# Optimization experiments

Measured on AMD Instinct MI355X. Metric: run time of the kernel, lower is better.

The kernel has to match this reference:

```python
import jax, jax.numpy as jnp
import numpy as np

B, K, D, H, T, S = 8192, 32, 768, 256, 16, 2  # batch, candidates, d_model, hidden, topics, shots
MAX_SHOT = 8
TEMP = 0.1


def _l2n(x, eps=1e-12):
    return x / jnp.clip(jnp.linalg.norm(x, axis=-1, keepdims=True), eps)


def setup_inputs() -> dict:
    key = jax.random.key(0)
    ks = jax.random.split(key, 20)
    f32 = jnp.float32
    rn = lambda k, shape, s: jax.random.normal(k, shape, f32) * s
    inp = {}
    inp['query_emb'] = jax.random.normal(ks[0], (B, D), f32)
    inp['cand_emb'] = jax.random.normal(ks[1], (B, K, D), f32)
    inp['W_in'] = rn(ks[2], (H, D), 0.03)              # input_proj (bias=False)
    inp['Wq_a'] = rn(ks[3], (H, H), 0.05)              # MHA in-proj q
    inp['Wk_a'] = rn(ks[4], (H, H), 0.05)
    inp['Wv_a'] = rn(ks[5], (H, H), 0.05)
    inp['bq_a'] = jnp.zeros((H,), f32)
    inp['bk_a'] = jnp.zeros((H,), f32)
    inp['bv_a'] = jnp.zeros((H,), f32)
    inp['Wo_a'] = rn(ks[6], (H, H), 0.05)              # MHA out-proj
    inp['bo_a'] = jnp.zeros((H,), f32)
    inp['ln_w'] = jnp.ones((H,), f32)
    inp['ln_b'] = jnp.zeros((H,), f32)
    inp['Wq'] = jnp.eye(H, dtype=f32) + rn(ks[7], (H, H), 0.01)   # query_proj (eye init + noise)
    inp['Wc'] = jnp.eye(H, dtype=f32) + rn(ks[8], (H, H), 0.01)   # cand_proj
    inp['W_ih'] = rn(ks[9], (3 * H, H), 0.05)          # GRUCell ih (r,z,n)
    inp['W_hh'] = rn(ks[10], (3 * H, H), 0.05)
    inp['b_ih'] = jnp.zeros((3 * H,), f32)
    inp['b_hh'] = jnp.zeros((3 * H,), f32)
    inp['step_emb'] = rn(ks[11], (MAX_SHOT, H), 0.02)
    inp['topic_protos'] = rn(ks[12], (T, H), 0.02)
    inp['Wqt'] = rn(ks[13], (T, H), 0.05)              # query_topic_head
    inp['bqt'] = jnp.zeros((T,), f32)
    inp['cover_lambda'] = jnp.array(-2.0, f32)
    return inp


def reference(query_emb, cand_emb, W_in, Wq_a, Wk_a, Wv_a, bq_a, bk_a, bv_a,
              Wo_a, bo_a, ln_w, ln_b, Wq, Wc, W_ih, W_hh, b_ih, b_hh,
              step_emb, topic_protos, Wqt, bqt, cover_lambda):
    Bd = query_emb.shape[0]
    # input projection 768 -> 256
    qr = query_emb @ W_in.T                                # [B,H]
    cr = jnp.einsum('bkd,hd->bkh', cand_emb, W_in)         # [B,K,H]
    # single-head cross-attention (query len 1, eval mode -> no dropout)
    q = qr @ Wq_a.T + bq_a
    k = jnp.einsum('bkh,gh->bkg', cr, Wk_a) + bk_a
    v = jnp.einsum('bkh,gh->bkg', cr, Wv_a) + bv_a
    attn = jax.nn.softmax(jnp.einsum('bh,bkh->bk', q, k) / jnp.sqrt(jnp.float32(H)))
    ctx = jnp.einsum('bk,bkh->bh', attn, v) @ Wo_a.T + bo_a
    # residual + LayerNorm
    x = ctx + qr
    mu = jnp.mean(x, -1, keepdims=True)
    var = jnp.var(x, -1, keepdims=True)
    qe = (x - mu) / jnp.sqrt(var + 1e-5) * ln_w + ln_b
    # pointer projections + L2 normalize
    h = _l2n(qe @ Wq.T)                                    # [B,H]
    cn = _l2n(jnp.einsum('bkh,gh->bkg', cr, Wc))           # [B,K,H]
    topic_probs = jax.nn.softmax(jnp.einsum('bkh,th->bkt', cn, _l2n(topic_protos)))  # [B,K,T]
    need = jax.nn.softmax(h @ Wqt.T + bqt)                 # [B,T]
    lam = jax.nn.softplus(cover_lambda)
    sel = jnp.zeros((Bd, K), bool)
    covered = jnp.zeros((Bd, T), jnp.float32)
    rows = jnp.arange(Bd)
    logits, preds = [], []
    for step in range(S):
        h_step = _l2n(h + step_emb[min(step, MAX_SHOT - 1)])
        scores = jnp.einsum('bh,bkh->bk', h_step, cn) / TEMP
        if step > 0:
            uncov = jnp.clip(1.0 - covered, 0.0, 1.0)
            gain = jnp.einsum('bt,bkt->bk', need * uncov, topic_probs)
            scores = scores + lam * gain
        scores = jnp.where(sel, -100.0, scores)
        logits.append(scores)
        idx = jnp.argmax(scores, axis=-1)                  # labels=None -> greedy feedback
        preds.append(idx)
        sel = sel.at[rows, idx].set(True)
        chosen = cn[rows, idx]                             # [B,H]
        covered = jnp.minimum(covered + topic_probs[rows, idx], 1.0)
        # GRUCell update
        gi = chosen @ W_ih.T + b_ih
        gh = h @ W_hh.T + b_hh
        ir, iz, ig = jnp.split(gi, 3, axis=-1)
        hr, hz, hg = jnp.split(gh, 3, axis=-1)
        r = jax.nn.sigmoid(ir + hr)
        z = jax.nn.sigmoid(iz + hz)
        n = jnp.tanh(ig + r * hg)
        h = _l2n((1.0 - z) * n + z * h)
    return jnp.stack(logits, 1), jnp.stack(preds, 1)       # [B,S,K], [B,S]
```

## Files before the change

### kernel.cpp

```cpp
#include <hip/hip_runtime.h>
#include <math.h>

#define B_ 8192
#define K_ 32
#define D_ 768
#define H_ 256
#define T_ 16
#define S_ 2

typedef unsigned int uint;
typedef unsigned short ushort;
typedef __attribute__((ext_vector_type(8))) short bf16x8;
typedef __attribute__((ext_vector_type(4))) float f32x4;

__device__ __forceinline__ float wsum(float v) {
  v += __shfl_xor(v, 32); v += __shfl_xor(v, 16); v += __shfl_xor(v, 8);
  v += __shfl_xor(v, 4);  v += __shfl_xor(v, 2);  v += __shfl_xor(v, 1);
  return v;
}
__device__ __forceinline__ float wmaxr(float v) {
  v = fmaxf(v, __shfl_xor(v, 32)); v = fmaxf(v, __shfl_xor(v, 16));
  v = fmaxf(v, __shfl_xor(v, 8));  v = fmaxf(v, __shfl_xor(v, 4));
  v = fmaxf(v, __shfl_xor(v, 2));  v = fmaxf(v, __shfl_xor(v, 1));
  return v;
}

__device__ __forceinline__ void split4(const float4 f, uint2& h, uint2& lo) {
  const uint ux = __float_as_uint(f.x), uy = __float_as_uint(f.y);
  const uint uz = __float_as_uint(f.z), uw = __float_as_uint(f.w);
  h.x = (uy & 0xFFFF0000u) | (ux >> 16);
  h.y = (uw & 0xFFFF0000u) | (uz >> 16);
  const float rx = f.x - __uint_as_float(ux & 0xFFFF0000u);
  const float ry = f.y - __uint_as_float(uy & 0xFFFF0000u);
  const float rz = f.z - __uint_as_float(uz & 0xFFFF0000u);
  const float rw = f.w - __uint_as_float(uw & 0xFFFF0000u);
  lo.x = (__float_as_uint(ry) & 0xFFFF0000u) | (__float_as_uint(rx) >> 16);
  lo.y = (__float_as_uint(rw) & 0xFFFF0000u) | (__float_as_uint(rz) >> 16);
}

__device__ __forceinline__ float dot4(const float4 a, const float4 b) {
  float s = a.x * b.x;
  s = fmaf(a.y, b.y, s); s = fmaf(a.z, b.z, s); s = fmaf(a.w, b.w, s);
  return s;
}


__global__ __launch_bounds__(256)
void fold_kernel(const float* __restrict__ Wk_a, const float* __restrict__ Wv_a,
                 const float* __restrict__ Wc,  const float* __restrict__ W_in,
                 float* __restrict__ WkinT, float* __restrict__ Wv_in,
                 ushort* __restrict__ Bh, ushort* __restrict__ Bl)
{
  const int i = blockIdx.x;
  const int m = blockIdx.y;
  const float* Wx = (m == 0) ? Wk_a : ((m == 1) ? Wv_a : Wc);
  const int t = threadIdx.x;
  float a0 = 0.f, a1 = 0.f, a2 = 0.f;
  for (int k = 0; k < H_; k++) {
    const float wv = Wx[i * H_ + k];
    const float* row = W_in + (size_t)k * D_;
    a0 = fmaf(wv, row[t], a0);
    a1 = fmaf(wv, row[t + 256], a1);
    a2 = fmaf(wv, row[t + 512], a2);
  }
  if (m == 0) {
    WkinT[(size_t)t * H_ + i] = a0;
    WkinT[(size_t)(t + 256) * H_ + i] = a1;
    WkinT[(size_t)(t + 512) * H_ + i] = a2;
  } else if (m == 1) {
    float* o = Wv_in + (size_t)i * D_;
    o[t] = a0; o[t + 256] = a1; o[t + 512] = a2;
  } else {
    const float vals[3] = {a0, a1, a2};
#pragma unroll
    for (int j = 0; j < 3; j++) {
      const int k = t + j * 256;
      const float v = vals[j];
      const int idx = (((k >> 5) * 16 + (i >> 4)) * 64 + ((i & 15) | (((k >> 3) & 3) << 4))) * 8 + (k & 7);
      const uint u = __float_as_uint(v);
      Bh[idx] = (ushort)(u >> 16);
      const float rr = v - __uint_as_float(u & 0xFFFF0000u);
      Bl[idx] = (ushort)(__float_as_uint(rr) >> 16);
    }
  }
}

struct TileJob { const float* W; ushort* Bh; ushort* Bl; int NB; int K; int rows; };
struct TileJobs { TileJob j[6]; };

__global__ __launch_bounds__(256)
void tile_all(TileJobs jobs)
{
  const TileJob J = jobs.j[blockIdx.y];
  const int n = blockIdx.x;
  if (n >= J.rows) return;
  const int t = threadIdx.x;
  for (int k = t; k < J.K; k += 256) {
    const float v = J.W[(size_t)n * J.K + k];
    const int idx = (((k >> 5) * J.NB + (n >> 4)) * 64 + ((n & 15) | (((k >> 3) & 3) << 4))) * 8 + (k & 7);
    const uint u = __float_as_uint(v);
    J.Bh[idx] = (ushort)(u >> 16);
    const float rr = v - __uint_as_float(u & 0xFFFF0000u);
    J.Bl[idx] = (ushort)(__float_as_uint(rr) >> 16);
  }
}

__global__ __launch_bounds__(256)
void proto_kernel(const float* __restrict__ tpro, float* __restrict__ pro)
{
  const int w = threadIdx.x >> 6, l = threadIdx.x & 63;
  for (int r = w; r < T_; r += 4) {
    const float4 v = *(const float4*)(tpro + (size_t)r * H_ + l * 4);
    const float n = fmaxf(sqrtf(wsum(v.x * v.x + v.y * v.y + v.z * v.z + v.w * v.w)), 1e-12f);
    float4 o; o.x = v.x / n; o.y = v.y / n; o.z = v.z / n; o.w = v.w / n;
    *(float4*)(pro + (size_t)r * H_ + l * 4) = o;
  }
}

__global__ __launch_bounds__(256)
void fold2_kernel(const float* __restrict__ Wq_a, const float* __restrict__ bq_a,
                  const float* __restrict__ bk_a, const float* __restrict__ Wo_a,
                  const float* __restrict__ bo_a, const float* __restrict__ bv_a,
                  const float* __restrict__ Wq,   const float* __restrict__ ln_w,
                  const float* __restrict__ ln_b, const float* __restrict__ WkinT,
                  const float* __restrict__ Wv_in,
                  float* __restrict__ Bqk, float* __restrict__ bqk,
                  float* __restrict__ Wvo, float* __restrict__ bvo,
                  float* __restrict__ Wqp, float* __restrict__ bqp,
                  float* __restrict__ vqbk, float* __restrict__ qcst)
{
  __shared__ float rd_s[4];
  const int n = blockIdx.x, t = threadIdx.x, w = t >> 6, l = t & 63;
  float s = 0.f;
  for (int hh = 0; hh < H_; hh++)
    s = fmaf(Wq_a[hh * H_ + t], WkinT[(size_t)n * H_ + hh], s);
  Bqk[(size_t)n * H_ + t] = s;
  float p = bq_a[t] * WkinT[(size_t)n * H_ + t];
  p = wsum(p);
  if (l == 0) rd_s[w] = p;
  __syncthreads();
  if (t == 0) bqk[n] = rd_s[0] + rd_s[1] + rd_s[2] + rd_s[3];
  if (n < H_) {
    float a0 = 0.f, a1 = 0.f, a2 = 0.f;
    for (int hh = 0; hh < H_; hh++) {
      const float wo = Wo_a[n * H_ + hh];
      const float* rowv = Wv_in + (size_t)hh * D_;
      a0 = fmaf(wo, rowv[t], a0);
      a1 = fmaf(wo, rowv[t + 256], a1);
      a2 = fmaf(wo, rowv[t + 512], a2);
    }
    Wvo[(size_t)n * D_ + t] = a0;
    Wvo[(size_t)n * D_ + t + 256] = a1;
    Wvo[(size_t)n * D_ + t + 512] = a2;
    float pb = Wo_a[n * H_ + t] * bv_a[t];
    pb = wsum(pb);
    __syncthreads();
    if (l == 0) rd_s[w] = pb;
    __syncthreads();
    if (t == 0) bvo[n] = rd_s[0] + rd_s[1] + rd_s[2] + rd_s[3] + bo_a[n];
    Wqp[n * H_ + t] = Wq[n * H_ + t] * ln_w[t];
    float pq = Wq[n * H_ + t] * ln_b[t];
    pq = wsum(pq);
    __syncthreads();
    if (l == 0) rd_s[w] = pq;
    __syncthreads();
    if (t == 0) bqp[n] = rd_s[0] + rd_s[1] + rd_s[2] + rd_s[3];
  }
  if (n == 0) {
    float sv = 0.f;
    for (int hh = 0; hh < H_; hh++) sv = fmaf(bk_a[hh], Wq_a[hh * H_ + t], sv);
    vqbk[t] = sv;
    float pc = bq_a[t] * bk_a[t];
    pc = wsum(pc);
    __syncthreads();
    if (l == 0) rd_s[w] = pc;
    __syncthreads();
    if (t == 0) qcst[0] = rd_s[0] + rd_s[1] + rd_s[2] + rd_s[3];
  }
}

__global__ __launch_bounds__(256, 3)
void gemm_cn_attn(const float* __restrict__ A, const ushort* __restrict__ Bh,
                  const ushort* __restrict__ Bl, const float* __restrict__ qkv,
                  const float* __restrict__ qr, const float* __restrict__ vqbk,
                  const float* __restrict__ qcst, float* __restrict__ C,
                  float* __restrict__ wce)
{
  __shared__ __align__(16) ushort AhS[2][2048], AlS[2][2048];
  __shared__ __align__(16) float4 qkv_s[384];
  __shared__ float sc_s[64], at_s[64], qbk_s[2];
  __shared__ float rsq[64][4];
  const int t = threadIdx.x, l = t & 63, w = t >> 6;
  const int r = t >> 2, kc = t & 3;
  const int tb = t >> 7;
  const float* Ag = A + ((size_t)blockIdx.x * 64 + r) * 768 + kc * 8;
  const int aslot = ((r >> 4) * 64 + ((r & 15) | (kc << 4))) * 8;
  const ushort* Bhb = Bh + ((w * 4) * 64 + l) * 8;
  const ushort* Blb = Bl + ((w * 4) * 64 + l) * 8;

  for (int i = t; i < 384; i += 256)
    qkv_s[i] = ((const float4*)qkv)[(size_t)blockIdx.x * 384 + i];
  if (w < 2) {
    const float4 q4 = ((const float4*)qr)[((size_t)blockIdx.x * 2 + w) * 64 + l];
    const float4 v4 = ((const float4*)vqbk)[l];
    float p = wsum(dot4(q4, v4));
    if (l == 0) qbk_s[w] = p + qcst[0];
  }

  f32x4 acc[4][4];
#pragma unroll
  for (int i = 0; i < 4; i++)
#pragma unroll
    for (int j = 0; j < 4; j++) acc[i][j] = (f32x4)0.f;

  float sc = 0.f;
  float4 f0 = *(const float4*)(Ag);
  float4 f1 = *(const float4*)(Ag + 4);
  __syncthreads();
  sc += dot4(f0, qkv_s[tb * 192 + kc * 2]) + dot4(f1, qkv_s[tb * 192 + kc * 2 + 1]);
  {
    uint2 ha, la, hb, lb;
    split4(f0, ha, la); split4(f1, hb, lb);
    *(uint4*)&AhS[0][aslot] = make_uint4(ha.x, ha.y, hb.x, hb.y);
    *(uint4*)&AlS[0][aslot] = make_uint4(la.x, la.y, lb.x, lb.y);
  }
  f0 = *(const float4*)(Ag + 32);
  f1 = *(const float4*)(Ag + 36);
  __syncthreads();

#pragma unroll 2
  for (int ks = 0; ks < 24; ks++) {
    const int cur = ks & 1;
    uint4 bhv[4], blv[4];
#pragma unroll
    for (int ni = 0; ni < 4; ni++) {
      bhv[ni] = *(const uint4*)(Bhb + ks * 8192 + ni * 512);
      blv[ni] = *(const uint4*)(Blb + ks * 8192 + ni * 512);
    }
    if (ks < 23) {
      sc += dot4(f0, qkv_s[tb * 192 + (ks + 1) * 8 + kc * 2]) +
            dot4(f1, qkv_s[tb * 192 + (ks + 1) * 8 + kc * 2 + 1]);
      uint2 ha, la, hb, lb;
      split4(f0, ha, la); split4(f1, hb, lb);
      *(uint4*)&AhS[cur ^ 1][aslot] = make_uint4(ha.x, ha.y, hb.x, hb.y);
      *(uint4*)&AlS[cur ^ 1][aslot] = make_uint4(la.x, la.y, lb.x, lb.y);
      if (ks < 22) {
        f0 = *(const float4*)(Ag + (ks + 2) * 32);
        f1 = *(const float4*)(Ag + (ks + 2) * 32 + 4);
      }
    }
#pragma unroll
    for (int mi = 0; mi < 4; mi++) {
      const bf16x8 ah = *(const bf16x8*)&AhS[cur][(mi * 64 + l) * 8];
      const bf16x8 al = *(const bf16x8*)&AlS[cur][(mi * 64 + l) * 8];
#pragma unroll
      for (int ni = 0; ni < 4; ni++) {
        const bf16x8 bhf = *(const bf16x8*)&bhv[ni];
        const bf16x8 blf = *(const bf16x8*)&blv[ni];
        acc[mi][ni] = __builtin_amdgcn_mfma_f32_16x16x32_bf16(ah, bhf, acc[mi][ni], 0, 0, 0);
        acc[mi][ni] = __builtin_amdgcn_mfma_f32_16x16x32_bf16(al, bhf, acc[mi][ni], 0, 0, 0);
        acc[mi][ni] = __builtin_amdgcn_mfma_f32_16x16x32_bf16(ah, blf, acc[mi][ni], 0, 0, 0);
      }
    }
    __syncthreads();
  }

  sc += __shfl_xor(sc, 1);
  sc += __shfl_xor(sc, 2);
  if ((t & 3) == 0) sc_s[r] = sc;
  __syncthreads();
  if (w < 2) {
    float s = (l < 32) ? (sc_s[w * 32 + l] + qbk_s[w]) * (1.f / 16.f) : -1e30f;
    const float m = wmaxr(s);
    const float e = (l < 32) ? expf(s - m) : 0.f;
    const float su = wsum(e);
    if (l < 32) at_s[w * 32 + l] = e / su;
  }
  __syncthreads();
#pragma unroll
  for (int p = 0; p < 2; p++) {
    const int slot = t + p * 256;
    if (slot < 384) {
      const int tb2 = slot >= 192;
      const int idx = slot - tb2 * 192;
      const float4* cb = (const float4*)A + ((size_t)blockIdx.x * 64 + tb2 * 32) * 192 + idx;
      float4 a = make_float4(0.f, 0.f, 0.f, 0.f);
#pragma unroll 4
      for (int c = 0; c < 32; c++) {
        const float av = at_s[tb2 * 32 + c];
        const float4 f = cb[c * 192];
        a.x = fmaf(av, f.x, a.x); a.y = fmaf(av, f.y, a.y);
        a.z = fmaf(av, f.z, a.z); a.w = fmaf(av, f.w, a.w);
      }
      ((float4*)wce)[((size_t)blockIdx.x * 2 + tb2) * 192 + idx] = a;
    }
  }

#pragma unroll
  for (int mi = 0; mi < 4; mi++)
#pragma unroll
    for (int rg = 0; rg < 4; rg++) {
      float p = 0.f;
#pragma unroll
      for (int ni = 0; ni < 4; ni++) { const float v = acc[mi][ni][rg]; p = fmaf(v, v, p); }
      p += __shfl_xor(p, 1); p += __shfl_xor(p, 2); p += __shfl_xor(p, 4); p += __shfl_xor(p, 8);
      if ((l & 15) == 0) rsq[mi * 16 + (l >> 4) * 4 + rg][w] = p;
    }
  __syncthreads();
  const size_t row0 = (size_t)blockIdx.x * 64;
#pragma unroll
  for (int mi = 0; mi < 4; mi++)
#pragma unroll
    for (int rg = 0; rg < 4; rg++) {
      const int rl = mi * 16 + (l >> 4) * 4 + rg;
      const float ssum = rsq[rl][0] + rsq[rl][1] + rsq[rl][2] + rsq[rl][3];
      const float inv = 1.f / fmaxf(sqrtf(ssum), 1e-12f);
#pragma unroll
      for (int ni = 0; ni < 4; ni++)
        C[(row0 + rl) * H_ + w * 64 + ni * 16 + (l & 15)] = acc[mi][ni][rg] * inv;
    }
}

__global__ __launch_bounds__(256)
void tp_kernel(const float* __restrict__ cn, const float* __restrict__ pro,
               float* __restrict__ tp)
{
  __shared__ float cn_s[16][260];
  __shared__ float pro_s[16][260];
  const int t = threadIdx.x;
  const size_t row0 = (size_t)blockIdx.x * 16;
  const int sr = t >> 4;
#pragma unroll
  for (int j = 0; j < 4; j++) {
    const int c = (t & 15) * 4 + j * 64;
    *(float4*)&cn_s[sr][c] = *(const float4*)(cn + (row0 + sr) * H_ + c);
    *(float4*)&pro_s[sr][c] = *(const float4*)(pro + sr * H_ + c);
  }
  __syncthreads();
  const int r = t >> 4, tt = t & 15;
  float d = 0.f;
#pragma unroll 8
  for (int j = 0; j < 64; j++) {
    const float4 a = *(const float4*)&cn_s[r][j * 4];
    const float4 p = *(const float4*)&pro_s[tt][j * 4];
    d = fmaf(a.x, p.x, d); d = fmaf(a.y, p.y, d);
    d = fmaf(a.z, p.z, d); d = fmaf(a.w, p.w, d);
  }
  float m = d;
  m = fmaxf(m, __shfl_xor(m, 1)); m = fmaxf(m, __shfl_xor(m, 2));
  m = fmaxf(m, __shfl_xor(m, 4)); m = fmaxf(m, __shfl_xor(m, 8));
  const float e = expf(d - m);
  float su = e;
  su += __shfl_xor(su, 1); su += __shfl_xor(su, 2);
  su += __shfl_xor(su, 4); su += __shfl_xor(su, 8);
  tp[(row0 + r) * T_ + tt] = e / su;
}

template<int NKS, int NB, bool BIAS>
__global__ __launch_bounds__(256)
void gemm_bf(const float* __restrict__ A, const ushort* __restrict__ Bh,
             const ushort* __restrict__ Bl, const float* __restrict__ bias,
             float* __restrict__ C)
{
  __shared__ __align__(16) ushort AhS[2][4096], AlS[2][4096];
  const int t = threadIdx.x, l = t & 63, w = t >> 6;
  const int wr = w >> 1, wc = w & 1;
  const int Kd = NKS * 32, N = NB * 16;
  const int r = t >> 1, kc0 = (t & 1) * 2;
  const float* Ag = A + ((size_t)blockIdx.x * 128 + r) * Kd + kc0 * 8;
  const int aslot0 = ((r >> 4) * 64 + ((r & 15) | (kc0 << 4))) * 8;
  const int aslot1 = aslot0 + 128;
  const int nb0 = blockIdx.y * 4 + wc * 2;
  const ushort* Bhb = Bh + (nb0 * 64 + l) * 8;
  const ushort* Blb = Bl + (nb0 * 64 + l) * 8;

  f32x4 acc[4][2];
#pragma unroll
  for (int i = 0; i < 4; i++)
#pragma unroll
    for (int j = 0; j < 2; j++) acc[i][j] = (f32x4)0.f;

  float4 f0 = *(const float4*)(Ag);
  float4 f1 = *(const float4*)(Ag + 4);
  float4 f2 = *(const float4*)(Ag + 8);
  float4 f3 = *(const float4*)(Ag + 12);
  {
    uint2 ha, la, hb, lb;
    split4(f0, ha, la); split4(f1, hb, lb);
    *(uint4*)&AhS[0][aslot0] = make_uint4(ha.x, ha.y, hb.x, hb.y);
    *(uint4*)&AlS[0][aslot0] = make_uint4(la.x, la.y, lb.x, lb.y);
    split4(f2, ha, la); split4(f3, hb, lb);
    *(uint4*)&AhS[0][aslot1] = make_uint4(ha.x, ha.y, hb.x, hb.y);
    *(uint4*)&AlS[0][aslot1] = make_uint4(la.x, la.y, lb.x, lb.y);
  }
  f0 = *(const float4*)(Ag + 32); f1 = *(const float4*)(Ag + 36);
  f2 = *(const float4*)(Ag + 40); f3 = *(const float4*)(Ag + 44);
  __syncthreads();

#pragma unroll 2
  for (int ks = 0; ks < NKS; ks++) {
    const int cur = ks & 1;
    if (ks < NKS - 1) {
      uint2 ha, la, hb, lb;
      split4(f0, ha, la); split4(f1, hb, lb);
      *(uint4*)&AhS[cur ^ 1][aslot0] = make_uint4(ha.x, ha.y, hb.x, hb.y);
      *(uint4*)&AlS[cur ^ 1][aslot0] = make_uint4(la.x, la.y, lb.x, lb.y);
      split4(f2, ha, la); split4(f3, hb, lb);
      *(uint4*)&AhS[cur ^ 1][aslot1] = make_uint4(ha.x, ha.y, hb.x, hb.y);
      *(uint4*)&AlS[cur ^ 1][aslot1] = make_uint4(la.x, la.y, lb.x, lb.y);
      if (ks < NKS - 2) {
        f0 = *(const float4*)(Ag + (ks + 2) * 32);
        f1 = *(const float4*)(Ag + (ks + 2) * 32 + 4);
        f2 = *(const float4*)(Ag + (ks + 2) * 32 + 8);
        f3 = *(const float4*)(Ag + (ks + 2) * 32 + 12);
      }
    }
#pragma unroll
    for (int mi = 0; mi < 4; mi++) {
      const bf16x8 ah = *(const bf16x8*)&AhS[cur][((wr * 4 + mi) * 64 + l) * 8];
      const bf16x8 al = *(const bf16x8*)&AlS[cur][((wr * 4 + mi) * 64 + l) * 8];
#pragma unroll
      for (int ni = 0; ni < 2; ni++) {
        const bf16x8 bhf = *(const bf16x8*)(Bhb + ks * (NB * 512) + ni * 512);
        const bf16x8 blf = *(const bf16x8*)(Blb + ks * (NB * 512) + ni * 512);
        acc[mi][ni] = __builtin_amdgcn_mfma_f32_16x16x32_bf16(ah, bhf, acc[mi][ni], 0, 0, 0);
        acc[mi][ni] = __builtin_amdgcn_mfma_f32_16x16x32_bf16(al, bhf, acc[mi][ni], 0, 0, 0);
        acc[mi][ni] = __builtin_amdgcn_mfma_f32_16x16x32_bf16(ah, blf, acc[mi][ni], 0, 0, 0);
      }
    }
    __syncthreads();
  }

  const size_t row0 = (size_t)blockIdx.x * 128 + wr * 64;
  const int col0 = blockIdx.y * 64 + wc * 32;
#pragma unroll
  for (int mi = 0; mi < 4; mi++)
#pragma unroll
    for (int ni = 0; ni < 2; ni++) {
      const int col = col0 + ni * 16 + (l & 15);
      const float bb = BIAS ? bias[col] : 0.f;
#pragma unroll
      for (int rg = 0; rg < 4; rg++) {
        const size_t row = row0 + mi * 16 + (l >> 4) * 4 + rg;
        C[row * N + col] = acc[mi][ni][rg] + bb;
      }
    }
}

__global__ __launch_bounds__(256)
void ln_kernel(const float* __restrict__ xin, const float* __restrict__ res,
               float* __restrict__ xhat)
{
  const int w = threadIdx.x >> 6, l = threadIdx.x & 63;
  const size_t r = (size_t)blockIdx.x * 4 + w;
  const float4 a = *(const float4*)(xin + r * H_ + l * 4);
  const float4 b = *(const float4*)(res + r * H_ + l * 4);
  const float x0 = a.x + b.x, x1 = a.y + b.y, x2 = a.z + b.z, x3 = a.w + b.w;
  const float mu = wsum(x0 + x1 + x2 + x3) * (1.f / H_);
  const float d0 = x0 - mu, d1 = x1 - mu, d2 = x2 - mu, d3 = x3 - mu;
  const float var = wsum(d0 * d0 + d1 * d1 + d2 * d2 + d3 * d3) * (1.f / H_);
  const float isd = 1.f / sqrtf(var + 1e-5f);
  float4 o;
  o.x = d0 * isd; o.y = d1 * isd; o.z = d2 * isd; o.w = d3 * isd;
  *(float4*)(xhat + r * H_ + l * 4) = o;
}

__global__ __launch_bounds__(256)
void h_post(const float* __restrict__ hraw, const float* __restrict__ Wqt,
            const float* __restrict__ bqt, float* __restrict__ h, float* __restrict__ need)
{
  __shared__ float wq_s[T_ * H_];
  for (int i = threadIdx.x; i < T_ * H_; i += 256) wq_s[i] = Wqt[i];
  const int w = threadIdx.x >> 6, l = threadIdx.x & 63;
  const size_t r = (size_t)blockIdx.x * 4 + w;
  const float4 v = *(const float4*)(hraw + r * H_ + l * 4);
  const float n = fmaxf(sqrtf(wsum(v.x * v.x + v.y * v.y + v.z * v.z + v.w * v.w)), 1e-12f);
  float4 hn; hn.x = v.x / n; hn.y = v.y / n; hn.z = v.z / n; hn.w = v.w / n;
  *(float4*)(h + r * H_ + l * 4) = hn;
  __syncthreads();
  float mine = 0.f;
  for (int tt = 0; tt < T_; tt++) {
    const float4 p4 = *(const float4*)(wq_s + tt * H_ + l * 4);
    float p = hn.x * p4.x + hn.y * p4.y + hn.z * p4.z + hn.w * p4.w;
    p = wsum(p);
    if (l == tt) mine = p + bqt[l];
  }
  float s = (l < T_) ? mine : -1e30f;
  const float m = wmaxr(s);
  const float e = (l < T_) ? expf(s - m) : 0.f;
  const float su = wsum(e);
  if (l < T_) need[r * T_ + l] = e / su;
}

template<int STEP>
__global__ __launch_bounds__(256)
void score_kernel(const float* __restrict__ h, const float* __restrict__ se,
                  const float* __restrict__ cn, const float* __restrict__ tp,
                  const float* __restrict__ need, const float* __restrict__ clam,
                  float* __restrict__ covered, int* __restrict__ sel,
                  float* __restrict__ chosen, float* __restrict__ logits,
                  float* __restrict__ preds)
{
  __shared__ __align__(16) float hs_s[H_];
  __shared__ float nu_s[T_];
  __shared__ float sc_s[K_];
  __shared__ float rd_s[4];
  __shared__ int idx_s;
  const int b = blockIdx.x, t = threadIdx.x;
  const int w = t >> 6, l = t & 63;

  const float hv = h[(size_t)b * H_ + t] + se[STEP * H_ + t];
  const float ss = wsum(hv * hv);
  if (l == 0) rd_s[w] = ss;
  if (STEP == 1 && t < T_)
    nu_s[t] = need[(size_t)b * T_ + t] * fminf(fmaxf(1.f - covered[(size_t)b * T_ + t], 0.f), 1.f);
  __syncthreads();
  const float n = fmaxf(sqrtf(rd_s[0] + rd_s[1] + rd_s[2] + rd_s[3]), 1e-12f);
  hs_s[t] = hv / n;
  __syncthreads();

  const float lam = log1pf(expf(clam[0]));
  const float4 hf = *(const float4*)(hs_s + l * 4);
#pragma unroll
  for (int cc = 0; cc < 8; cc++) {
    const int c = w * 8 + cc;
    const float4 cv = *(const float4*)(cn + ((size_t)b * K_ + c) * H_ + l * 4);
    float p = cv.x * hf.x + cv.y * hf.y + cv.z * hf.z + cv.w * hf.w;
    p = wsum(p);
    float s = p / 0.1f;
    if (STEP == 1) {
      float g = (l < T_) ? nu_s[l] * tp[((size_t)b * K_ + c) * T_ + l] : 0.f;
      g = wsum(g);
      s += lam * g;
      if (sel[(size_t)b * K_ + c]) s = -100.f;
    }
    if (l == 0) sc_s[c] = s;
  }
  __syncthreads();
  if (w == 0) {
    float s = (l < K_) ? sc_s[l] : -1e30f;
    int bi = (l < K_) ? l : K_;
#pragma unroll
    for (int o = 32; o; o >>= 1) {
      const float s2 = __shfl_xor(s, o);
      const int i2 = __shfl_xor(bi, o);
      if (s2 > s || (s2 == s && i2 < bi)) { s = s2; bi = i2; }
    }
    if (l == 0) idx_s = bi;
  }
  __syncthreads();
  const int idx = idx_s;
  if (t < K_) logits[(size_t)b * (S_ * K_) + STEP * K_ + t] = sc_s[t];
  if (t == 0) preds[(size_t)b * S_ + STEP] = (float)idx;
  if (STEP == 0) {
    if (t < K_) sel[(size_t)b * K_ + t] = (t == idx) ? 1 : 0;
    if (t < T_) covered[(size_t)b * T_ + t] = fminf(tp[((size_t)b * K_ + idx) * T_ + t], 1.f);
    chosen[(size_t)b * H_ + t] = cn[((size_t)b * K_ + idx) * H_ + t];
  }
}

__global__ __launch_bounds__(256)
void gru_kernel(const float* __restrict__ gi, const float* __restrict__ gh, float* __restrict__ h)
{
  __shared__ float rd_s[4];
  const int b = blockIdx.x, t = threadIdx.x, w = t >> 6, l = t & 63;
  const size_t o = (size_t)b * (3 * H_);
  const float ir = gi[o + t], iz = gi[o + 256 + t], ig = gi[o + 512 + t];
  const float hr = gh[o + t], hz = gh[o + 256 + t], hg = gh[o + 512 + t];
  const float hv = h[(size_t)b * H_ + t];
  const float r = 1.f / (1.f + expf(-(ir + hr)));
  const float z = 1.f / (1.f + expf(-(iz + hz)));
  const float nn = tanhf(ig + r * hg);
  const float x = (1.f - z) * nn + z * hv;
  const float ss = wsum(x * x);
  if (l == 0) rd_s[w] = ss;
  __syncthreads();
  const float n = fmaxf(sqrtf(rd_s[0] + rd_s[1] + rd_s[2] + rd_s[3]), 1e-12f);
  h[(size_t)b * H_ + t] = x / n;
}

extern "C" void kernel_launch(void* const* d_in, const int* in_sizes, int n_in,
                              void* d_out, int out_size, void* d_ws, size_t ws_size,
                              hipStream_t stream)
{
  const float* query_emb = (const float*)d_in[0];
  const float* cand_emb  = (const float*)d_in[1];
  const float* W_in = (const float*)d_in[2];
  const float* Wq_a = (const float*)d_in[3];
  const float* Wk_a = (const float*)d_in[4];
  const float* Wv_a = (const float*)d_in[5];
  const float* bq_a = (const float*)d_in[6];
  const float* bk_a = (const float*)d_in[7];
  const float* bv_a = (const float*)d_in[8];
  const float* Wo_a = (const float*)d_in[9];
  const float* bo_a = (const float*)d_in[10];
  const float* ln_w = (const float*)d_in[11];
  const float* ln_b = (const float*)d_in[12];
  const float* Wq   = (const float*)d_in[13];
  const float* Wc   = (const float*)d_in[14];
  const float* W_ih = (const float*)d_in[15];
  const float* W_hh = (const float*)d_in[16];
  const float* b_ih = (const float*)d_in[17];
  const float* b_hh = (const float*)d_in[18];
  const float* step_emb = (const float*)d_in[19];
  const float* tpro = (const float*)d_in[20];
  const float* Wqt  = (const float*)d_in[21];
  const float* bqt  = (const float*)d_in[22];
  const float* clam = (const float*)d_in[23];

  float* ws = (float*)d_ws;
  size_t o = 0;
  float* WkinT = ws + o; o += (size_t)D_ * H_;
  float* Wv_in = ws + o; o += (size_t)H_ * D_;
  ushort* BhW  = (ushort*)(ws + o); o += 98304;
  ushort* BlW  = (ushort*)(ws + o); o += 98304;
  float* pro   = ws + o; o += (size_t)T_ * H_;
  float* Bqk   = ws + o; o += (size_t)D_ * H_;
  float* bqk   = ws + o; o += 1024;
  float* Wvo   = ws + o; o += (size_t)H_ * D_;
  float* bvo   = ws + o; o += 256;
  float* Wqp   = ws + o; o += (size_t)H_ * H_;
  float* bqp   = ws + o; o += 256;
  float* vqbk  = ws + o; o += 256;
  float* qcst  = ws + o; o += 4;
  ushort* WintH = (ushort*)(ws + o); o += 98304;
  ushort* WintL = (ushort*)(ws + o); o += 98304;
  ushort* BqktH = (ushort*)(ws + o); o += 98304;
  ushort* BqktL = (ushort*)(ws + o); o += 98304;
  ushort* WvotH = (ushort*)(ws + o); o += 98304;
  ushort* WvotL = (ushort*)(ws + o); o += 98304;
  ushort* WqptH = (ushort*)(ws + o); o += 32768;
  ushort* WqptL = (ushort*)(ws + o); o += 32768;
  ushort* WihtH = (ushort*)(ws + o); o += 98304;
  ushort* WihtL = (ushort*)(ws + o); o += 98304;
  ushort* WhhtH = (ushort*)(ws + o); o += 98304;
  ushort* WhhtL = (ushort*)(ws + o); o += 98304;
  float* qr    = ws + o; o += (size_t)B_ * H_;
  float* qkv   = ws + o; o += (size_t)B_ * D_;
  float* wce   = ws + o; o += (size_t)B_ * D_;
  float* ctxb  = ws + o; o += (size_t)B_ * H_;
  float* xhat  = ws + o; o += (size_t)B_ * H_;
  float* h     = ws + o; o += (size_t)B_ * H_;
  float* need  = ws + o; o += (size_t)B_ * T_;
  float* cn    = ws + o; o += (size_t)B_ * K_ * H_;
  float* tp    = ws + o; o += (size_t)B_ * K_ * T_;
  int*   sel   = (int*)(ws + o); o += (size_t)B_ * K_;
  float* cov   = ws + o; o += (size_t)B_ * T_;
  float* chosen= ws + o; o += (size_t)B_ * H_;

  float* out_logits = (float*)d_out;
  float* out_preds  = (float*)d_out + (size_t)B_ * S_ * K_;

  fold_kernel<<<dim3(H_, 3), 256, 0, stream>>>(Wk_a, Wv_a, Wc, W_in, WkinT, Wv_in, BhW, BlW);
  proto_kernel<<<1, 256, 0, stream>>>(tpro, pro);
  fold2_kernel<<<D_, 256, 0, stream>>>(Wq_a, bq_a, bk_a, Wo_a, bo_a, bv_a, Wq, ln_w, ln_b,
                                       WkinT, Wv_in, Bqk, bqk, Wvo, bvo, Wqp, bqp, vqbk, qcst);
  TileJobs jobs;
  jobs.j[0] = {W_in, WintH, WintL, 16, 768, 256};
  jobs.j[1] = {Bqk,  BqktH, BqktL, 48, 256, 768};
  jobs.j[2] = {Wvo,  WvotH, WvotL, 16, 768, 256};
  jobs.j[3] = {Wqp,  WqptH, WqptL, 16, 256, 256};
  jobs.j[4] = {W_ih, WihtH, WihtL, 48, 256, 768};
  jobs.j[5] = {W_hh, WhhtH, WhhtL, 48, 256, 768};
  tile_all<<<dim3(768, 6), 256, 0, stream>>>(jobs);

  gemm_bf<24, 16, false><<<dim3(B_ / 128, 4), 256, 0, stream>>>(query_emb, WintH, WintL, nullptr, qr);
  gemm_bf<8, 48, true><<<dim3(B_ / 128, 12), 256, 0, stream>>>(qr, BqktH, BqktL, bqk, qkv);

  gemm_cn_attn<<<(B_ * K_) / 64, 256, 0, stream>>>(cand_emb, BhW, BlW, qkv, qr, vqbk, qcst, cn, wce);

  gemm_bf<24, 16, true><<<dim3(B_ / 128, 4), 256, 0, stream>>>(wce, WvotH, WvotL, bvo, ctxb);
  ln_kernel<<<B_ / 4, 256, 0, stream>>>(ctxb, qr, xhat);
  gemm_bf<8, 16, true><<<dim3(B_ / 128, 4), 256, 0, stream>>>(xhat, WqptH, WqptL, bqp, ctxb);
  h_post<<<B_ / 4, 256, 0, stream>>>(ctxb, Wqt, bqt, h, need);

  tp_kernel<<<(B_ * K_) / 16, 256, 0, stream>>>(cn, pro, tp);

  score_kernel<0><<<B_, 256, 0, stream>>>(h, step_emb, cn, tp, need, clam, cov, sel, chosen, out_logits, out_preds);
  gemm_bf<8, 48, true><<<dim3(B_ / 128, 12), 256, 0, stream>>>(chosen, WihtH, WihtL, b_ih, qkv);
  gemm_bf<8, 48, true><<<dim3(B_ / 128, 12), 256, 0, stream>>>(h, WhhtH, WhhtL, b_hh, wce);
  gru_kernel<<<B_, 256, 0, stream>>>(qkv, wce, h);
  score_kernel<1><<<B_, 256, 0, stream>>>(h, step_emb, cn, tp, need, clam, cov, sel, chosen, out_logits, out_preds);
}
```

Baseline: 892.9 us.

## Fuse ctx GEMM with LayerNorm, GRU into step-1 scoring, and inline topic probabilities

```diff
diff --git a/kernel.cpp b/kernel.cpp
--- a/kernel.cpp
+++ b/kernel.cpp
@@ -321,39 +321,106 @@
     }
 }
 
-__global__ __launch_bounds__(256)
-void tp_kernel(const float* __restrict__ cn, const float* __restrict__ pro,
-               float* __restrict__ tp)
-{
-  __shared__ float cn_s[16][260];
-  __shared__ float pro_s[16][260];
-  const int t = threadIdx.x;
-  const size_t row0 = (size_t)blockIdx.x * 16;
-  const int sr = t >> 4;
-#pragma unroll
-  for (int j = 0; j < 4; j++) {
-    const int c = (t & 15) * 4 + j * 64;
-    *(float4*)&cn_s[sr][c] = *(const float4*)(cn + (row0 + sr) * H_ + c);
-    *(float4*)&pro_s[sr][c] = *(const float4*)(pro + sr * H_ + c);
-  }
-  __syncthreads();
-  const int r = t >> 4, tt = t & 15;
-  float d = 0.f;
-#pragma unroll 8
-  for (int j = 0; j < 64; j++) {
-    const float4 a = *(const float4*)&cn_s[r][j * 4];
-    const float4 p = *(const float4*)&pro_s[tt][j * 4];
-    d = fmaf(a.x, p.x, d); d = fmaf(a.y, p.y, d);
-    d = fmaf(a.z, p.z, d); d = fmaf(a.w, p.w, d);
-  }
-  float m = d;
-  m = fmaxf(m, __shfl_xor(m, 1)); m = fmaxf(m, __shfl_xor(m, 2));
-  m = fmaxf(m, __shfl_xor(m, 4)); m = fmaxf(m, __shfl_xor(m, 8));
-  const float e = expf(d - m);
-  float su = e;
-  su += __shfl_xor(su, 1); su += __shfl_xor(su, 2);
-  su += __shfl_xor(su, 4); su += __shfl_xor(su, 8);
-  tp[(row0 + r) * T_ + tt] = e / su;
+__global__ __launch_bounds__(256, 3)
+void gemm_ctx_ln(const float* __restrict__ A, const ushort* __restrict__ Bh,
+                 const ushort* __restrict__ Bl, const float* __restrict__ bvo,
+                 const float* __restrict__ qr, float* __restrict__ xhat)
+{
+  __shared__ __align__(16) ushort AhS[2][2048], AlS[2][2048];
+  __shared__ float red[64][4][2];
+  const int t = threadIdx.x, l = t & 63, w = t >> 6;
+  const int r = t >> 2, kc = t & 3;
+  const float* Ag = A + ((size_t)blockIdx.x * 64 + r) * 768 + kc * 8;
+  const int aslot = ((r >> 4) * 64 + ((r & 15) | (kc << 4))) * 8;
+  const ushort* Bhb = Bh + ((w * 4) * 64 + l) * 8;
+  const ushort* Blb = Bl + ((w * 4) * 64 + l) * 8;
+
+  f32x4 acc[4][4];
+#pragma unroll
+  for (int i = 0; i < 4; i++)
+#pragma unroll
+    for (int j = 0; j < 4; j++) acc[i][j] = (f32x4)0.f;
+
+  float4 f0 = *(const float4*)(Ag);
+  float4 f1 = *(const float4*)(Ag + 4);
+  {
+    uint2 ha, la, hb, lb;
+    split4(f0, ha, la); split4(f1, hb, lb);
+    *(uint4*)&AhS[0][aslot] = make_uint4(ha.x, ha.y, hb.x, hb.y);
+    *(uint4*)&AlS[0][aslot] = make_uint4(la.x, la.y, lb.x, lb.y);
+  }
+  f0 = *(const float4*)(Ag + 32);
+  f1 = *(const float4*)(Ag + 36);
+  __syncthreads();
+
+#pragma unroll 2
+  for (int ks = 0; ks < 24; ks++) {
+    const int cur = ks & 1;
+    uint4 bhv[4], blv[4];
+#pragma unroll
+    for (int ni = 0; ni < 4; ni++) {
+      bhv[ni] = *(const uint4*)(Bhb + ks * 8192 + ni * 512);
+      blv[ni] = *(const uint4*)(Blb + ks * 8192 + ni * 512);
+    }
+    if (ks < 23) {
+      uint2 ha, la, hb, lb;
+      split4(f0, ha, la); split4(f1, hb, lb);
+      *(uint4*)&AhS[cur ^ 1][aslot] = make_uint4(ha.x, ha.y, hb.x, hb.y);
+      *(uint4*)&AlS[cur ^ 1][aslot] = make_uint4(la.x, la.y, lb.x, lb.y);
+      if (ks < 22) {
+        f0 = *(const float4*)(Ag + (ks + 2) * 32);
+        f1 = *(const float4*)(Ag + (ks + 2) * 32 + 4);
+      }
+    }
+#pragma unroll
+    for (int mi = 0; mi < 4; mi++) {
+      const bf16x8 ah = *(const bf16x8*)&AhS[cur][(mi * 64 + l) * 8];
+      const bf16x8 al = *(const bf16x8*)&AlS[cur][(mi * 64 + l) * 8];
+#pragma unroll
+      for (int ni = 0; ni < 4; ni++) {
+        const bf16x8 bhf = *(const bf16x8*)&bhv[ni];
+        const bf16x8 blf = *(const bf16x8*)&blv[ni];
+        acc[mi][ni] = __builtin_amdgcn_mfma_f32_16x16x32_bf16(ah, bhf, acc[mi][ni], 0, 0, 0);
+        acc[mi][ni] = __builtin_amdgcn_mfma_f32_16x16x32_bf16(al, bhf, acc[mi][ni], 0, 0, 0);
+        acc[mi][ni] = __builtin_amdgcn_mfma_f32_16x16x32_bf16(ah, blf, acc[mi][ni], 0, 0, 0);
+      }
+    }
+    __syncthreads();
+  }
+
+  const size_t row0 = (size_t)blockIdx.x * 64;
+#pragma unroll
+  for (int mi = 0; mi < 4; mi++)
+#pragma unroll
+    for (int rg = 0; rg < 4; rg++) {
+      const int rl = mi * 16 + (l >> 4) * 4 + rg;
+      float sx = 0.f, sxx = 0.f;
+#pragma unroll
+      for (int ni = 0; ni < 4; ni++) {
+        const int col = w * 64 + ni * 16 + (l & 15);
+        const float x = acc[mi][ni][rg] + bvo[col] + qr[(row0 + rl) * H_ + col];
+        acc[mi][ni][rg] = x;
+        sx += x; sxx = fmaf(x, x, sxx);
+      }
+      sx += __shfl_xor(sx, 1); sx += __shfl_xor(sx, 2); sx += __shfl_xor(sx, 4); sx += __shfl_xor(sx, 8);
+      sxx += __shfl_xor(sxx, 1); sxx += __shfl_xor(sxx, 2); sxx += __shfl_xor(sxx, 4); sxx += __shfl_xor(sxx, 8);
+      if ((l & 15) == 0) { red[rl][w][0] = sx; red[rl][w][1] = sxx; }
+    }
+  __syncthreads();
+#pragma unroll
+  for (int mi = 0; mi < 4; mi++)
+#pragma unroll
+    for (int rg = 0; rg < 4; rg++) {
+      const int rl = mi * 16 + (l >> 4) * 4 + rg;
+      const float SX = red[rl][0][0] + red[rl][1][0] + red[rl][2][0] + red[rl][3][0];
+      const float SXX = red[rl][0][1] + red[rl][1][1] + red[rl][2][1] + red[rl][3][1];
+      const float mu = SX * (1.f / H_);
+      const float var = SXX * (1.f / H_) - mu * mu;
+      const float isd = 1.f / sqrtf(var + 1e-5f);
+#pragma unroll
+      for (int ni = 0; ni < 4; ni++)
+        xhat[(row0 + rl) * H_ + w * 64 + ni * 16 + (l & 15)] = (acc[mi][ni][rg] - mu) * isd;
+    }
 }
 
 template<int NKS, int NB, bool BIAS>
@@ -448,24 +515,6 @@
 }
 
 __global__ __launch_bounds__(256)
-void ln_kernel(const float* __restrict__ xin, const float* __restrict__ res,
-               float* __restrict__ xhat)
-{
-  const int w = threadIdx.x >> 6, l = threadIdx.x & 63;
-  const size_t r = (size_t)blockIdx.x * 4 + w;
-  const float4 a = *(const float4*)(xin + r * H_ + l * 4);
-  const float4 b = *(const float4*)(res + r * H_ + l * 4);
-  const float x0 = a.x + b.x, x1 = a.y + b.y, x2 = a.z + b.z, x3 = a.w + b.w;
-  const float mu = wsum(x0 + x1 + x2 + x3) * (1.f / H_);
-  const float d0 = x0 - mu, d1 = x1 - mu, d2 = x2 - mu, d3 = x3 - mu;
-  const float var = wsum(d0 * d0 + d1 * d1 + d2 * d2 + d3 * d3) * (1.f / H_);
-  const float isd = 1.f / sqrtf(var + 1e-5f);
-  float4 o;
-  o.x = d0 * isd; o.y = d1 * isd; o.z = d2 * isd; o.w = d3 * isd;
-  *(float4*)(xhat + r * H_ + l * 4) = o;
-}
-
-__global__ __launch_bounds__(256)
 void h_post(const float* __restrict__ hraw, const float* __restrict__ Wqt,
             const float* __restrict__ bqt, float* __restrict__ h, float* __restrict__ need)
 {
@@ -492,49 +541,36 @@
   if (l < T_) need[r * T_ + l] = e / su;
 }
 
-template<int STEP>
 __global__ __launch_bounds__(256)
-void score_kernel(const float* __restrict__ h, const float* __restrict__ se,
-                  const float* __restrict__ cn, const float* __restrict__ tp,
-                  const float* __restrict__ need, const float* __restrict__ clam,
-                  float* __restrict__ covered, int* __restrict__ sel,
-                  float* __restrict__ chosen, float* __restrict__ logits,
-                  float* __restrict__ preds)
+void score0_kernel(const float* __restrict__ h, const float* __restrict__ se,
+                   const float* __restrict__ cn, const float* __restrict__ pro,
+                   float* __restrict__ covered, float* __restrict__ chosen,
+                   float* __restrict__ logits, float* __restrict__ preds)
 {
   __shared__ __align__(16) float hs_s[H_];
-  __shared__ float nu_s[T_];
+  __shared__ __align__(16) float cr_s[H_];
+  __shared__ float part_s[T_ * 16];
   __shared__ float sc_s[K_];
   __shared__ float rd_s[4];
   __shared__ int idx_s;
   const int b = blockIdx.x, t = threadIdx.x;
   const int w = t >> 6, l = t & 63;
 
-  const float hv = h[(size_t)b * H_ + t] + se[STEP * H_ + t];
+  const float hv = h[(size_t)b * H_ + t] + se[t];
   const float ss = wsum(hv * hv);
   if (l == 0) rd_s[w] = ss;
-  if (STEP == 1 && t < T_)
-    nu_s[t] = need[(size_t)b * T_ + t] * fminf(fmaxf(1.f - covered[(size_t)b * T_ + t], 0.f), 1.f);
   __syncthreads();
   const float n = fmaxf(sqrtf(rd_s[0] + rd_s[1] + rd_s[2] + rd_s[3]), 1e-12f);
   hs_s[t] = hv / n;
   __syncthreads();
 
-  const float lam = log1pf(expf(clam[0]));
   const float4 hf = *(const float4*)(hs_s + l * 4);
 #pragma unroll
   for (int cc = 0; cc < 8; cc++) {
     const int c = w * 8 + cc;
     const float4 cv = *(const float4*)(cn + ((size_t)b * K_ + c) * H_ + l * 4);
-    float p = cv.x * hf.x + cv.y * hf.y + cv.z * hf.z + cv.w * hf.w;
-    p = wsum(p);
-    float s = p / 0.1f;
-    if (STEP == 1) {
-      float g = (l < T_) ? nu_s[l] * tp[((size_t)b * K_ + c) * T_ + l] : 0.f;
-      g = wsum(g);
-      s += lam * g;
-      if (sel[(size_t)b * K_ + c]) s = -100.f;
-    }
-    if (l == 0) sc_s[c] = s;
+    float p = wsum(dot4(cv, hf));
+    if (l == 0) sc_s[c] = p * 10.f;
   }
   __syncthreads();
   if (w == 0) {
@@ -550,33 +586,135 @@
   }
   __syncthreads();
   const int idx = idx_s;
-  if (t < K_) logits[(size_t)b * (S_ * K_) + STEP * K_ + t] = sc_s[t];
-  if (t == 0) preds[(size_t)b * S_ + STEP] = (float)idx;
-  if (STEP == 0) {
-    if (t < K_) sel[(size_t)b * K_ + t] = (t == idx) ? 1 : 0;
-    if (t < T_) covered[(size_t)b * T_ + t] = fminf(tp[((size_t)b * K_ + idx) * T_ + t], 1.f);
-    chosen[(size_t)b * H_ + t] = cn[((size_t)b * K_ + idx) * H_ + t];
+  if (t < K_) logits[(size_t)b * (S_ * K_) + t] = sc_s[t];
+  if (t == 0) preds[(size_t)b * S_] = (float)idx;
+
+  const float crv = cn[((size_t)b * K_ + idx) * H_ + t];
+  cr_s[t] = crv;
+  chosen[(size_t)b * H_ + t] = crv;
+  __syncthreads();
+  {
+    const int tt = t & 15, ch = t >> 4;
+    float p = 0.f;
+#pragma unroll
+    for (int j = 0; j < 16; j++)
+      p = fmaf(cr_s[ch * 16 + j], pro[tt * H_ + ch * 16 + j], p);
+    part_s[tt * 16 + ch] = p;
+  }
+  __syncthreads();
+  if (t < 16) {
+    float d = 0.f;
+#pragma unroll
+    for (int ch = 0; ch < 16; ch++) d += part_s[t * 16 + ch];
+    float mx = d;
+    mx = fmaxf(mx, __shfl_xor(mx, 1)); mx = fmaxf(mx, __shfl_xor(mx, 2));
+    mx = fmaxf(mx, __shfl_xor(mx, 4)); mx = fmaxf(mx, __shfl_xor(mx, 8));
+    const float e = expf(d - mx);
+    float su = e;
+    su += __shfl_xor(su, 1); su += __shfl_xor(su, 2);
+    su += __shfl_xor(su, 4); su += __shfl_xor(su, 8);
+    covered[(size_t)b * T_ + t] = fminf(e / su, 1.f);
   }
 }
 
 __global__ __launch_bounds__(256)
-void gru_kernel(const float* __restrict__ gi, const float* __restrict__ gh, float* __restrict__ h)
-{
-  __shared__ float rd_s[4];
-  const int b = blockIdx.x, t = threadIdx.x, w = t >> 6, l = t & 63;
+void score1_kernel(const float* __restrict__ gi, const float* __restrict__ gh,
+                   const float* __restrict__ h,  const float* __restrict__ se,
+                   const float* __restrict__ cn, const float* __restrict__ pro,
+                   const float* __restrict__ need, const float* __restrict__ clam,
+                   const float* __restrict__ covered,
+                   float* __restrict__ logits, float* __restrict__ preds)
+{
+  __shared__ __align__(16) float cn_s[K_ * 260];
+  __shared__ __align__(16) float pro_s[T_ * 260];
+  __shared__ __align__(16) float hs_s[H_];
+  __shared__ float gd_s[K_ * T_];
+  __shared__ float gain_s[K_];
+  __shared__ float nu_s[T_], sc_s[K_], rd_s[4], rd2_s[4];
+  const int b = blockIdx.x, t = threadIdx.x;
+  const int w = t >> 6, l = t & 63;
+
   const size_t o = (size_t)b * (3 * H_);
   const float ir = gi[o + t], iz = gi[o + 256 + t], ig = gi[o + 512 + t];
   const float hr = gh[o + t], hz = gh[o + 256 + t], hg = gh[o + 512 + t];
   const float hv = h[(size_t)b * H_ + t];
-  const float r = 1.f / (1.f + expf(-(ir + hr)));
-  const float z = 1.f / (1.f + expf(-(iz + hz)));
-  const float nn = tanhf(ig + r * hg);
-  const float x = (1.f - z) * nn + z * hv;
+  const float rr = 1.f / (1.f + expf(-(ir + hr)));
+  const float zz = 1.f / (1.f + expf(-(iz + hz)));
+  const float nn = tanhf(ig + rr * hg);
+  const float x = (1.f - zz) * nn + zz * hv;
   const float ss = wsum(x * x);
   if (l == 0) rd_s[w] = ss;
-  __syncthreads();
-  const float n = fmaxf(sqrtf(rd_s[0] + rd_s[1] + rd_s[2] + rd_s[3]), 1e-12f);
-  h[(size_t)b * H_ + t] = x / n;
+
+  {
+    const float4* cng = (const float4*)(cn + (size_t)b * K_ * H_);
+    float4* cns4 = (float4*)cn_s;
+    for (int i = t; i < 2048; i += 256) cns4[(i >> 6) * 65 + (i & 63)] = cng[i];
+    const float4* prg = (const float4*)pro;
+    float4* prs4 = (float4*)pro_s;
+    for (int i = t; i < 1024; i += 256) prs4[(i >> 6) * 65 + (i & 63)] = prg[i];
+  }
+  if (t < T_)
+    nu_s[t] = need[(size_t)b * T_ + t] * fminf(fmaxf(1.f - covered[(size_t)b * T_ + t], 0.f), 1.f);
+  __syncthreads();
+  const float n1 = fmaxf(sqrtf(rd_s[0] + rd_s[1] + rd_s[2] + rd_s[3]), 1e-12f);
+  const float y = x / n1 + se[H_ + t];
+  const float ss2 = wsum(y * y);
+  if (l == 0) rd2_s[w] = ss2;
+  __syncthreads();
+  const float n2 = fmaxf(sqrtf(rd2_s[0] + rd2_s[1] + rd2_s[2] + rd2_s[3]), 1e-12f);
+  hs_s[t] = y / n2;
+  __syncthreads();
+
+  const float4* cn_s4 = (const float4*)cn_s;
+  const float4* pro_s4 = (const float4*)pro_s;
+  const float4 hf = *(const float4*)(hs_s + l * 4);
+#pragma unroll
+  for (int cc = 0; cc < 8; cc++) {
+    const int c = w * 8 + cc;
+    const float4 cv = cn_s4[c * 65 + l];
+    float p = wsum(dot4(cv, hf));
+    if (l == 0) sc_s[c] = p * 10.f;
+  }
+#pragma unroll
+  for (int pr = 0; pr < 2; pr++) {
+    const int idx2 = t + pr * 256;
+    const int c = idx2 >> 4, tt = idx2 & 15;
+    float d = 0.f;
+#pragma unroll 8
+    for (int j = 0; j < 64; j++)
+      d += dot4(cn_s4[c * 65 + j], pro_s4[tt * 65 + j]);
+    gd_s[idx2] = d;
+  }
+  __syncthreads();
+  if (t < K_) {
+    float mx = -1e30f;
+#pragma unroll
+    for (int tt = 0; tt < T_; tt++) mx = fmaxf(mx, gd_s[t * T_ + tt]);
+    float su = 0.f, ga = 0.f;
+#pragma unroll
+    for (int tt = 0; tt < T_; tt++) {
+      const float e = expf(gd_s[t * T_ + tt] - mx);
+      su += e; ga = fmaf(nu_s[tt], e, ga);
+    }
+    gain_s[t] = ga / su;
+  }
+  const int i0 = (int)preds[(size_t)b * S_];
+  __syncthreads();
+  if (w == 0) {
+    const float lam = log1pf(expf(clam[0]));
+    float s = (l < K_) ? sc_s[l] + lam * gain_s[l] : -1e30f;
+    if (l < K_ && l == i0) s = -100.f;
+    if (l < K_) logits[(size_t)b * (S_ * K_) + K_ + l] = s;
+    int bi = (l < K_) ? l : K_;
+    float sm = s;
+#pragma unroll
+    for (int o2 = 32; o2; o2 >>= 1) {
+      const float s2 = __shfl_xor(sm, o2);
+      const int i2 = __shfl_xor(bi, o2);
+      if (s2 > sm || (s2 == sm && i2 < bi)) { sm = s2; bi = i2; }
+    }
+    if (l == 0) preds[(size_t)b * S_ + 1] = (float)bi;
+  }
 }
 
 extern "C" void kernel_launch(void* const* d_in, const int* in_sizes, int n_in,
@@ -643,8 +781,6 @@
   float* h     = ws + o; o += (size_t)B_ * H_;
   float* need  = ws + o; o += (size_t)B_ * T_;
   float* cn    = ws + o; o += (size_t)B_ * K_ * H_;
-  float* tp    = ws + o; o += (size_t)B_ * K_ * T_;
-  int*   sel   = (int*)(ws + o); o += (size_t)B_ * K_;
   float* cov   = ws + o; o += (size_t)B_ * T_;
   float* chosen= ws + o; o += (size_t)B_ * H_;
 
@@ -669,16 +805,13 @@
 
   gemm_cn_attn<<<(B_ * K_) / 64, 256, 0, stream>>>(cand_emb, BhW, BlW, qkv, qr, vqbk, qcst, cn, wce);
 
-  gemm_bf<24, 16, true><<<dim3(B_ / 128, 4), 256, 0, stream>>>(wce, WvotH, WvotL, bvo, ctxb);
-  ln_kernel<<<B_ / 4, 256, 0, stream>>>(ctxb, qr, xhat);
+  gemm_ctx_ln<<<B_ / 64, 256, 0, stream>>>(wce, WvotH, WvotL, bvo, qr, xhat);
   gemm_bf<8, 16, true><<<dim3(B_ / 128, 4), 256, 0, stream>>>(xhat, WqptH, WqptL, bqp, ctxb);
   h_post<<<B_ / 4, 256, 0, stream>>>(ctxb, Wqt, bqt, h, need);
 
-  tp_kernel<<<(B_ * K_) / 16, 256, 0, stream>>>(cn, pro, tp);
-
-  score_kernel<0><<<B_, 256, 0, stream>>>(h, step_emb, cn, tp, need, clam, cov, sel, chosen, out_logits, out_preds);
+  score0_kernel<<<B_, 256, 0, stream>>>(h, step_emb, cn, pro, cov, chosen, out_logits, out_preds);
   gemm_bf<8, 48, true><<<dim3(B_ / 128, 12), 256, 0, stream>>>(chosen, WihtH, WihtL, b_ih, qkv);
   gemm_bf<8, 48, true><<<dim3(B_ / 128, 12), 256, 0, stream>>>(h, WhhtH, WhhtL, b_hh, wce);
-  gru_kernel<<<B_, 256, 0, stream>>>(qkv, wce, h);
-  score_kernel<1><<<B_, 256, 0, stream>>>(h, step_emb, cn, tp, need, clam, cov, sel, chosen, out_logits, out_preds);
-}
+  score1_kernel<<<B_, 256, 0, stream>>>(qkv, wce, h, step_emb, cn, pro, need, clam, cov,
+                                        out_logits, out_preds);
+}
```

Result: no change. 883.5 us, median of 2 (-1.1%).
